# Optimization experiments

Hardware: AMD Instinct MI355X
Metric: run time of the kernel (lower is better)

Reference implementation:

```python
import jax, jax.numpy as jnp
import numpy as np


def _qrnn_forward(X, W, b):
    seq_len, batch, d = X.shape
    H = W.shape[0] // 3
    Y = jnp.einsum('sbd,hd->sbh', X, W) + b  # [S,B,3H]
    Z, F, O = jnp.split(Y, 3, axis=2)
    Z = jnp.tanh(Z)
    F = jax.nn.sigmoid(F)

    # ForgetMult with hidden_init=None: h_0 = f_0*z_0; h_t = f_t*z_t + (1-f_t)*h_{t-1}
    # Equivalent to scan from h_{-1} = 0.
    def step(h_prev, fz):
        f_t, z_t = fz
        h = f_t * z_t + (1.0 - f_t) * h_prev
        return h, h

    h0 = jnp.zeros((batch, H), dtype=X.dtype)
    _, C = jax.lax.scan(step, h0, (F, Z))  # [S,B,H]
    Hout = jax.nn.sigmoid(O) * C
    return Hout, C[-1:, :, :]


def setup_inputs() -> dict:
    key = jax.random.key(0)
    k1, k2, k3 = jax.random.split(key, 3)
    S, B, D, Hdim = 1024, 16, 1024, 1024
    X = jax.random.normal(k1, (S, B, D), dtype=jnp.float32)
    W = jax.random.normal(k2, (3 * Hdim, D), dtype=jnp.float32) * (1.0 / np.sqrt(D))
    b = jax.random.normal(k3, (3 * Hdim,), dtype=jnp.float32) * 0.01
    return {"X": X, "W": W, "b": b}


def reference(X, W, b):
    return _qrnn_forward(X, W, b)
```

## Files before the change

kernel.cpp:

```cpp
#include <hip/hip_runtime.h>
#include <hip/hip_bf16.h>
#include <stdint.h>

typedef __bf16 bf16x8 __attribute__((ext_vector_type(8)));
typedef float f32x4 __attribute__((ext_vector_type(4)));

constexpr int S = 1024, Bsz = 16, Hd = 1024;
constexpr int M = S * Bsz;
constexpr int N = 3 * Hd;
constexpr int K = 1024;
constexpr int BM = 128, BN = 128, BK = 64;
constexpr int NCH = 64, CS = S / NCH;
constexpr int BH = Bsz * Hd;
constexpr int EP = 136;

__device__ __forceinline__ float fast_sigmoid(float x) { return 1.0f / (1.0f + __expf(-x)); }
__device__ __forceinline__ float fast_tanh(float x) { return 2.0f / (1.0f + __expf(-2.0f * x)) - 1.0f; }

__device__ __forceinline__ void gld_lds16(const __bf16* g, __bf16* l) {
  __builtin_amdgcn_global_load_lds(
      (const __attribute__((address_space(1))) void*)g,
      (__attribute__((address_space(3))) void*)l,
      16, 0, 0);
}

__global__ void convert_f32_bf16(const float* __restrict__ src, __bf16* __restrict__ dst, int n8) {
  int i = blockIdx.x * blockDim.x + threadIdx.x;
  if (i >= n8) return;
  const float4* s4 = (const float4*)src;
  float4 a = s4[2 * i], b = s4[2 * i + 1];
  bf16x8 v;
  v[0] = (__bf16)a.x; v[1] = (__bf16)a.y; v[2] = (__bf16)a.z; v[3] = (__bf16)a.w;
  v[4] = (__bf16)b.x; v[5] = (__bf16)b.y; v[6] = (__bf16)b.z; v[7] = (__bf16)b.w;
  *((bf16x8*)dst + i) = v;
}

__global__ __launch_bounds__(256) void gemm_act(const __bf16* __restrict__ A,
                                                const __bf16* __restrict__ Bw,
                                                const float* __restrict__ bias,
                                                __bf16* __restrict__ Y) {
  __shared__ __align__(16) __bf16 smem[BM * EP];
  __bf16* As = smem;
  __bf16* Bs = smem + BM * BK;
  const int t = threadIdx.x;
  const int lane = t & 63;
  const int wave = t >> 6;
  const int wm = wave >> 1, wn = wave & 1;
  const int bid = blockIdx.x;
  const int swz = (bid & 7) * (3072 / 8) + (bid >> 3);
  const int tn = swz % (N / BN);
  const int tm = swz / (N / BN);
  const int m0 = tm * BM, n0 = tn * BN;
  const int lrow = lane & 15;
  const int quad = lane >> 4;

  const int srow = t >> 3;
  const int scol = (t & 7) * 8;
  const __bf16* gA = A + (size_t)(m0 + srow) * K + scol;
  const __bf16* gB = Bw + (size_t)(n0 + srow) * K + scol;
  __bf16* lA = As + wave * 512;
  __bf16* lB = Bs + wave * 512;

  f32x4 acc[4][4] = {};

  for (int k0 = 0; k0 < K; k0 += BK) {
    __syncthreads();
#pragma unroll
    for (int i = 0; i < 4; ++i) {
      gld_lds16(gA + (size_t)i * 32 * K, lA + i * 2048);
      gld_lds16(gB + (size_t)i * 32 * K, lB + i * 2048);
    }
    gA += BK; gB += BK;
    __syncthreads();

#pragma unroll
    for (int kk = 0; kk < 2; ++kk) {
      bf16x8 af[4], bfr[4];
#pragma unroll
      for (int mi = 0; mi < 4; ++mi)
        af[mi] = *(const bf16x8*)(&As[(wm * 64 + mi * 16 + lrow) * BK + kk * 32 + quad * 8]);
#pragma unroll
      for (int ni = 0; ni < 4; ++ni)
        bfr[ni] = *(const bf16x8*)(&Bs[(wn * 64 + ni * 16 + lrow) * BK + kk * 32 + quad * 8]);
#pragma unroll
      for (int mi = 0; mi < 4; ++mi)
#pragma unroll
        for (int ni = 0; ni < 4; ++ni)
          acc[mi][ni] = __builtin_amdgcn_mfma_f32_16x16x32_bf16(af[mi], bfr[ni], acc[mi][ni], 0, 0, 0);
    }
  }

  __syncthreads();
#pragma unroll
  for (int ni = 0; ni < 4; ++ni) {
    int colL = wn * 64 + ni * 16 + lrow;
    int col = n0 + colL;
    float bv = bias[col];
    bool is_tanh = (col < Hd);
#pragma unroll
    for (int mi = 0; mi < 4; ++mi) {
#pragma unroll
      for (int r = 0; r < 4; ++r) {
        int rowL = wm * 64 + mi * 16 + quad * 4 + r;
        float y = acc[mi][ni][r] + bv;
        float v = is_tanh ? fast_tanh(y) : fast_sigmoid(y);
        smem[rowL * EP + colL] = (__bf16)v;
      }
    }
  }
  __syncthreads();
#pragma unroll
  for (int it = 0; it < 8; ++it) {
    int slot = it * 256 + t;
    int rowL = slot >> 4;
    int cw = slot & 15;
    bf16x8 vv = *(const bf16x8*)(&smem[rowL * EP + cw * 8]);
    *(bf16x8*)(&Y[(size_t)(m0 + rowL) * N + n0 + cw * 8]) = vv;
  }
}

__global__ __launch_bounds__(256) void scan_pass1(const __bf16* __restrict__ Y,
                                                  float* __restrict__ Ac,
                                                  float* __restrict__ Bc) {
  int tid = blockIdx.x * 256 + threadIdx.x;
  int c = tid >> 11;
  int r = tid & 2047;
  int bh0 = r << 3;
  int b = bh0 >> 10, h0 = bh0 & (Hd - 1);
  const size_t sstep = (size_t)Bsz * N;
  size_t base0 = (size_t)b * N + h0 + (size_t)(c * CS) * sstep;
  float A[8], Bv[8];
#pragma unroll
  for (int v = 0; v < 8; ++v) { A[v] = 1.0f; Bv[v] = 0.0f; }
#pragma unroll
  for (int j0 = 0; j0 < CS; j0 += 8) {
    bf16x8 zv[8], fv[8];
#pragma unroll
    for (int j = 0; j < 8; ++j) {
      size_t base = base0 + (size_t)(j0 + j) * sstep;
      zv[j] = *(const bf16x8*)(Y + base);
      fv[j] = *(const bf16x8*)(Y + base + Hd);
    }
#pragma unroll
    for (int j = 0; j < 8; ++j) {
#pragma unroll
      for (int v = 0; v < 8; ++v) {
        float z = (float)zv[j][v], f = (float)fv[j][v];
        float a = 1.0f - f;
        Bv[v] = fmaf(a, Bv[v], f * z);
        A[v] *= a;
      }
    }
  }
  int ob = c * BH + bh0;
  f32x4 a0, a1, b0, b1;
#pragma unroll
  for (int v = 0; v < 4; ++v) { a0[v] = A[v]; a1[v] = A[v + 4]; b0[v] = Bv[v]; b1[v] = Bv[v + 4]; }
  *(f32x4*)(Ac + ob) = a0;
  *(f32x4*)(Ac + ob + 4) = a1;
  *(f32x4*)(Bc + ob) = b0;
  *(f32x4*)(Bc + ob + 4) = b1;
}

__global__ __launch_bounds__(256) void scan_pass2(const float* __restrict__ Ac,
                                                  const float* __restrict__ Bc,
                                                  float* __restrict__ hin,
                                                  float* __restrict__ clast) {
  int bh = blockIdx.x * 256 + threadIdx.x;
  float h = 0.0f;
#pragma unroll 8
  for (int c = 0; c < NCH; ++c) {
    hin[c * BH + bh] = h;
    h = fmaf(Ac[c * BH + bh], h, Bc[c * BH + bh]);
  }
  clast[bh] = h;
}

__global__ __launch_bounds__(256) void scan_pass3(const __bf16* __restrict__ Y,
                                                  const float* __restrict__ hin,
                                                  float* __restrict__ hout) {
  int tid = blockIdx.x * 256 + threadIdx.x;
  int c = tid >> 11;
  int r = tid & 2047;
  int bh0 = r << 3;
  int b = bh0 >> 10, h0 = bh0 & (Hd - 1);
  const size_t sstep = (size_t)Bsz * N;
  size_t base0 = (size_t)b * N + h0 + (size_t)(c * CS) * sstep;
  size_t obase0 = (size_t)b * Hd + h0 + (size_t)(c * CS) * BH;
  float hp[8];
  {
    f32x4 h04 = *(const f32x4*)(hin + c * BH + bh0);
    f32x4 h14 = *(const f32x4*)(hin + c * BH + bh0 + 4);
#pragma unroll
    for (int v = 0; v < 4; ++v) { hp[v] = h04[v]; hp[v + 4] = h14[v]; }
  }
#pragma unroll
  for (int j0 = 0; j0 < CS; j0 += 8) {
    bf16x8 zv[8], fv[8], ov[8];
#pragma unroll
    for (int j = 0; j < 8; ++j) {
      size_t base = base0 + (size_t)(j0 + j) * sstep;
      zv[j] = *(const bf16x8*)(Y + base);
      fv[j] = *(const bf16x8*)(Y + base + Hd);
      ov[j] = *(const bf16x8*)(Y + base + 2 * Hd);
    }
#pragma unroll
    for (int j = 0; j < 8; ++j) {
      f32x4 o0, o1;
#pragma unroll
      for (int v = 0; v < 8; ++v) {
        float z = (float)zv[j][v], f = (float)fv[j][v], o = (float)ov[j][v];
        hp[v] = fmaf(f, z - hp[v], hp[v]);
        float out = o * hp[v];
        if (v < 4) o0[v] = out; else o1[v - 4] = out;
      }
      size_t ob = obase0 + (size_t)(j0 + j) * BH;
      *(f32x4*)(hout + ob) = o0;
      *(f32x4*)(hout + ob + 4) = o1;
    }
  }
}

extern "C" void kernel_launch(void* const* d_in, const int* in_sizes, int n_in,
                              void* d_out, int out_size, void* d_ws, size_t ws_size,
                              hipStream_t stream) {
  const float* X = (const float*)d_in[0];
  const float* W = (const float*)d_in[1];
  const float* bias = (const float*)d_in[2];
  float* out = (float*)d_out;

  char* ws = (char*)d_ws;
  __bf16* Xb = (__bf16*)ws;
  __bf16* Wb = (__bf16*)(ws + 33554432);
  __bf16* Yv = (__bf16*)(ws + 39845888);
  float* Ac = (float*)(ws + 39845888 + 100663296);
  float* Bc = Ac + NCH * BH;
  float* hin = Bc + NCH * BH;

  convert_f32_bf16<<<8192, 256, 0, stream>>>(X, Xb, 2097152);
  convert_f32_bf16<<<1536, 256, 0, stream>>>(W, Wb, 393216);

  dim3 ggrid((M / BM) * (N / BN));
  dim3 vgrid(NCH * BH / 8 / 256);
  gemm_act<<<ggrid, 256, 0, stream>>>(Xb, Wb, bias, Yv);
  scan_pass1<<<vgrid, 256, 0, stream>>>(Yv, Ac, Bc);
  scan_pass2<<<BH / 256, 256, 0, stream>>>(Ac, Bc, hin, out + 16777216);
  scan_pass3<<<vgrid, 256, 0, stream>>>(Yv, hin, out);
}
```

Measured before the change: 345.2 us.

## XOR-swizzle GEMM LDS tiles, merge conversion kernels, drop block swizzle

Applies an XOR swizzle to the 16-byte column groups when the GEMM loads A and B tiles into LDS, and uses the matching swizzle on the fragment reads, to cut LDS bank conflicts on the MFMA operand loads. It also fuses the two f32-to-bf16 conversion kernels into a single launch to save one launch. The blockIdx-to-tile swizzle is removed in favour of plain row-major tile order, which can change L2 reuse of the A and B operands.

```diff
diff --git a/kernel.cpp b/kernel.cpp
--- a/kernel.cpp
+++ b/kernel.cpp
@@ -24,15 +24,18 @@
       16, 0, 0);
 }
 
-__global__ void convert_f32_bf16(const float* __restrict__ src, __bf16* __restrict__ dst, int n8) {
+__global__ void convert_all(const float* __restrict__ X, const float* __restrict__ W,
+                            __bf16* __restrict__ Xb, __bf16* __restrict__ Wb) {
   int i = blockIdx.x * blockDim.x + threadIdx.x;
-  if (i >= n8) return;
+  const float* src; __bf16* dst; int idx;
+  if (i < 2097152) { src = X; dst = Xb; idx = i; }
+  else             { src = W; dst = Wb; idx = i - 2097152; }
   const float4* s4 = (const float4*)src;
-  float4 a = s4[2 * i], b = s4[2 * i + 1];
+  float4 a = s4[2 * idx], b = s4[2 * idx + 1];
   bf16x8 v;
   v[0] = (__bf16)a.x; v[1] = (__bf16)a.y; v[2] = (__bf16)a.z; v[3] = (__bf16)a.w;
   v[4] = (__bf16)b.x; v[5] = (__bf16)b.y; v[6] = (__bf16)b.z; v[7] = (__bf16)b.w;
-  *((bf16x8*)dst + i) = v;
+  *((bf16x8*)dst + idx) = v;
 }
 
 __global__ __launch_bounds__(256) void gemm_act(const __bf16* __restrict__ A,
@@ -41,23 +44,22 @@
                                                 __bf16* __restrict__ Y) {
   __shared__ __align__(16) __bf16 smem[BM * EP];
   __bf16* As = smem;
-  __bf16* Bs = smem + BM * BK;
+  __bf16* Bs = smem + 8192;
   const int t = threadIdx.x;
   const int lane = t & 63;
   const int wave = t >> 6;
   const int wm = wave >> 1, wn = wave & 1;
-  const int bid = blockIdx.x;
-  const int swz = (bid & 7) * (3072 / 8) + (bid >> 3);
-  const int tn = swz % (N / BN);
-  const int tm = swz / (N / BN);
+  const int tn = blockIdx.x % (N / BN);
+  const int tm = blockIdx.x / (N / BN);
   const int m0 = tm * BM, n0 = tn * BN;
   const int lrow = lane & 15;
   const int quad = lane >> 4;
+  const int l7 = lrow & 7;
 
   const int srow = t >> 3;
-  const int scol = (t & 7) * 8;
-  const __bf16* gA = A + (size_t)(m0 + srow) * K + scol;
-  const __bf16* gB = Bw + (size_t)(n0 + srow) * K + scol;
+  const int sg = (t & 7) ^ (srow & 7);
+  const __bf16* gA = A + (size_t)(m0 + srow) * K + sg * 8;
+  const __bf16* gB = Bw + (size_t)(n0 + srow) * K + sg * 8;
   __bf16* lA = As + wave * 512;
   __bf16* lB = Bs + wave * 512;
 
@@ -75,13 +77,14 @@
 
 #pragma unroll
     for (int kk = 0; kk < 2; ++kk) {
+      const int gsw = ((kk * 4 + quad) ^ l7) * 8;
       bf16x8 af[4], bfr[4];
 #pragma unroll
       for (int mi = 0; mi < 4; ++mi)
-        af[mi] = *(const bf16x8*)(&As[(wm * 64 + mi * 16 + lrow) * BK + kk * 32 + quad * 8]);
+        af[mi] = *(const bf16x8*)(&As[(wm * 64 + mi * 16 + lrow) * BK + gsw]);
 #pragma unroll
       for (int ni = 0; ni < 4; ++ni)
-        bfr[ni] = *(const bf16x8*)(&Bs[(wn * 64 + ni * 16 + lrow) * BK + kk * 32 + quad * 8]);
+        bfr[ni] = *(const bf16x8*)(&Bs[(wn * 64 + ni * 16 + lrow) * BK + gsw]);
 #pragma unroll
       for (int mi = 0; mi < 4; ++mi)
 #pragma unroll
@@ -237,8 +240,7 @@
   float* Bc = Ac + NCH * BH;
   float* hin = Bc + NCH * BH;
 
-  convert_f32_bf16<<<8192, 256, 0, stream>>>(X, Xb, 2097152);
-  convert_f32_bf16<<<1536, 256, 0, stream>>>(W, Wb, 393216);
+  convert_all<<<9728, 256, 0, stream>>>(X, W, Xb, Wb);
 
   dim3 ggrid((M / BM) * (N / BN));
   dim3 vgrid(NCH * BH / 8 / 256);
```

Result: faster. 304.3 us (median of 2 runs) (-11.9%).
